# Optimization experiments

Measured on AMD Instinct MI355X. Metric: run time of the kernel, lower is better.

The kernel has to match this reference:

```python
import jax, jax.numpy as jnp
import numpy as np

BN_EPS = 1e-5


def setup_inputs() -> dict:
    key = jax.random.key(0)
    ks = jax.random.split(key, 5)
    b, c, h, w = 4, 128, 64, 64
    x = jax.random.normal(ks[0], (b, c, h, w), dtype=jnp.float32)
    # conv1x1 c -> 2c (fan-in scaled)
    w_inp = jax.random.normal(ks[1], (2 * c, c), dtype=jnp.float32) / np.sqrt(c)
    b_inp = jax.random.normal(ks[2], (2 * c,), dtype=jnp.float32) * 0.01
    bn_gamma = jnp.ones((2 * c,), dtype=jnp.float32)
    bn_beta = jnp.zeros((2 * c,), dtype=jnp.float32)
    bn_mean = jnp.zeros((2 * c,), dtype=jnp.float32)
    bn_var = jnp.ones((2 * c,), dtype=jnp.float32)
    w_out = jax.random.normal(ks[3], (c, c), dtype=jnp.float32) / np.sqrt(c)
    b_out = jax.random.normal(ks[4], (c,), dtype=jnp.float32) * 0.01
    return {
        "x": x, "w_inp": w_inp, "b_inp": b_inp,
        "bn_gamma": bn_gamma, "bn_beta": bn_beta,
        "bn_mean": bn_mean, "bn_var": bn_var,
        "w_out": w_out, "b_out": b_out,
    }


def reference(x, w_inp, b_inp, bn_gamma, bn_beta, bn_mean, bn_var, w_out, b_out):
    b, c, h, w = x.shape
    scale = c ** (-0.5)
    # project_inp: conv1x1 (c -> 2c) + BatchNorm2d (eval mode, running stats)
    t = jnp.einsum('bchw,oc->bohw', x, w_inp) + b_inp[None, :, None, None]
    bn_scale = bn_gamma * jax.lax.rsqrt(bn_var + BN_EPS)
    t = t * bn_scale[None, :, None, None] + (bn_beta - bn_mean * bn_scale)[None, :, None, None]
    # split qv along channels, flatten spatial to tokens: [b, N, c], N = h*w
    q = t[:, :c].reshape(b, c, h * w).transpose(0, 2, 1)
    v = t[:, c:].reshape(b, c, h * w).transpose(0, 2, 1)
    # self-similarity attention on q: [b, N, N]
    atn = jax.nn.softmax(jnp.einsum('bnc,bmc->bnm', q, q) * scale, axis=-1)
    y = jnp.einsum('bnm,bmc->bnc', atn, v)  # [b, N, c]
    y = y.transpose(0, 2, 1).reshape(b, c, h, w)
    # project_out: conv1x1 c -> c
    y = jnp.einsum('bchw,oc->bohw', y, w_out) + b_out[None, :, None, None]
    return (y, atn)
```

## Files before the change

kernel.cpp:

```cpp
#include <hip/hip_runtime.h>
#include <stdint.h>
#include <math.h>

#define C_DIM 128
#define N_TOK 4096
#define NB 4
#define LOG2E 1.4426950408889634f

typedef __attribute__((ext_vector_type(8))) short bf16x8;
typedef __attribute__((ext_vector_type(4))) short bf16x4;
typedef __attribute__((ext_vector_type(4))) float f32x4;

__device__ __forceinline__ unsigned short f2bf(float f) {
  unsigned u = __builtin_bit_cast(unsigned, f);
  unsigned r = (u + 0x7FFFu + ((u >> 16) & 1u)) >> 16;
  return (unsigned short)r;
}
__device__ __forceinline__ float bf2f(unsigned short h) {
  return __builtin_bit_cast(float, ((unsigned)h) << 16);
}
__device__ __forceinline__ void gload_lds16(const void* g, void* l) {
  __builtin_amdgcn_global_load_lds((const __attribute__((address_space(1))) void*)g,
                                   (__attribute__((address_space(3))) void*)l,
                                   16, 0, 0);
}

__global__ __launch_bounds__(256) void proj_in_kernel(
    const float* __restrict__ x, const float* __restrict__ w_inp,
    const float* __restrict__ b_inp, const float* __restrict__ gamma,
    const float* __restrict__ beta, const float* __restrict__ mean,
    const float* __restrict__ var,
    unsigned short* __restrict__ q, unsigned short* __restrict__ vT,
    int* __restrict__ m2bits) {
  __shared__ char smem[36096];
  unsigned short* xh = (unsigned short*)smem;
  unsigned short* xl = (unsigned short*)(smem + 17408);
  float* blkred = (float*)(smem + 35840);

  const int tid = threadIdx.x;
  const int b = blockIdx.x >> 6;
  const int n0 = (blockIdx.x & 63) << 6;
  const int lane = tid & 63;
  const int wave = tid >> 6;
  const int l15 = lane & 15, lg = lane >> 4;

  {
    const int c = tid >> 1;
    const int j0 = (tid & 1) * 32;
    const float* src = x + ((size_t)b * C_DIM + c) * N_TOK + n0 + j0;
#pragma unroll
    for (int j = 0; j < 32; j += 4) {
      float4 v4 = *(const float4*)(src + j);
#pragma unroll
      for (int e = 0; e < 4; e++) {
        float f = (&v4.x)[e];
        unsigned short hi = f2bf(f);
        unsigned short lo = f2bf(f - bf2f(hi));
        int n = j0 + j + e;
        xh[n * 136 + c] = hi;
        xl[n * 136 + c] = lo;
      }
    }
  }
  __syncthreads();

  f32x4 acc[4][4];
#pragma unroll
  for (int i = 0; i < 4; i++)
#pragma unroll
    for (int j = 0; j < 4; j++) acc[i][j] = {0.f, 0.f, 0.f, 0.f};

#pragma unroll
  for (int ks = 0; ks < 4; ks++) {
    bf16x8 ah[4], al[4];
#pragma unroll
    for (int ot = 0; ot < 4; ot++) {
      const int o = wave * 64 + ot * 16 + l15;
      const float* wp = w_inp + o * C_DIM + ks * 32 + lg * 8;
      float4 w0 = *(const float4*)wp;
      float4 w1 = *(const float4*)(wp + 4);
#pragma unroll
      for (int e = 0; e < 8; e++) {
        float f = (e < 4) ? (&w0.x)[e] : (&w1.x)[e - 4];
        unsigned short hi = f2bf(f);
        ah[ot][e] = (short)hi;
        al[ot][e] = (short)f2bf(f - bf2f(hi));
      }
    }
#pragma unroll
    for (int nt = 0; nt < 4; nt++) {
      const int off = (nt * 16 + l15) * 136 + ks * 32 + lg * 8;
      bf16x8 bh = *(const bf16x8*)(xh + off);
      bf16x8 bl = *(const bf16x8*)(xl + off);
#pragma unroll
      for (int ot = 0; ot < 4; ot++) {
        acc[ot][nt] = __builtin_amdgcn_mfma_f32_16x16x32_bf16(ah[ot], bh, acc[ot][nt], 0, 0, 0);
        acc[ot][nt] = __builtin_amdgcn_mfma_f32_16x16x32_bf16(ah[ot], bl, acc[ot][nt], 0, 0, 0);
        acc[ot][nt] = __builtin_amdgcn_mfma_f32_16x16x32_bf16(al[ot], bh, acc[ot][nt], 0, 0, 0);
      }
    }
  }
  __syncthreads();

  unsigned short* qT = (unsigned short*)smem;
  unsigned short* vTl = (unsigned short*)(smem + 17408);

#pragma unroll
  for (int ot = 0; ot < 4; ot++) {
#pragma unroll
    for (int r = 0; r < 4; r++) {
      const int o = wave * 64 + ot * 16 + lg * 4 + r;
      float A = gamma[o] * rsqrtf(var[o] + 1e-5f);
      float Bo = beta[o] + (b_inp[o] - mean[o]) * A;
#pragma unroll
      for (int nt = 0; nt < 4; nt++) {
        float val = acc[ot][nt][r] * A + Bo;
        unsigned short hv = f2bf(val);
        int n = nt * 16 + l15;
        if (wave < 2) {
          qT[n * 136 + o] = hv;
        } else {
          vTl[(o - 128) * 72 + n] = hv;
        }
      }
    }
  }
  __syncthreads();
  {
    int j = tid >> 2, c0 = (tid & 3) * 32;
    unsigned short* dst = q + ((size_t)b * N_TOK + n0 + j) * C_DIM + c0;
    const unsigned short* s = qT + j * 136 + c0;
#pragma unroll
    for (int i = 0; i < 32; i += 8) *(bf16x8*)(dst + i) = *(const bf16x8*)(s + i);
  }
  {
    int c = tid >> 1, h = (tid & 1) * 32;
    unsigned short* dst = vT + ((size_t)b * C_DIM + c) * N_TOK + n0 + h;
    const unsigned short* s = vTl + c * 72 + h;
#pragma unroll
    for (int i = 0; i < 32; i += 8) *(bf16x8*)(dst + i) = *(const bf16x8*)(s + i);
  }
  {
    int row = tid >> 2, qn = tid & 3;
    const unsigned short* qr = qT + row * 136 + qn * 32;
    float s = 0.f;
#pragma unroll
    for (int i = 0; i < 32; i++) {
      float f = bf2f(qr[i]);
      s = fmaf(f, f, s);
    }
    s += __shfl_xor(s, 1);
    s += __shfl_xor(s, 2);
    if ((tid & 3) == 0) blkred[row] = s;
    __syncthreads();
    if (tid < 64) {
      float v = blkred[tid];
      v = fmaxf(v, __shfl_xor(v, 1));
      v = fmaxf(v, __shfl_xor(v, 2));
      v = fmaxf(v, __shfl_xor(v, 4));
      v = fmaxf(v, __shfl_xor(v, 8));
      v = fmaxf(v, __shfl_xor(v, 16));
      v = fmaxf(v, __shfl_xor(v, 32));
      if (tid == 0) atomicMax(m2bits, __float_as_int(v));
    }
  }
}

__global__ __launch_bounds__(256) void attn_kernel(
    const unsigned short* __restrict__ q, const unsigned short* __restrict__ vT,
    const float* __restrict__ w_out, const float* __restrict__ b_out,
    float* __restrict__ yout, float* __restrict__ atn,
    const float* __restrict__ m2ptr) {
  __shared__ char smem[55552];

  const int tid = threadIdx.x;
  const int lane = tid & 63;
  const int wave = tid >> 6;
  const int rg = wave >> 1;
  const int kh = wave & 1;
  const int l15 = lane & 15, lg = lane >> 4, l7 = lane & 7;
  const int b = blockIdx.x >> 7;
  const int q0 = (blockIdx.x & 127) << 5;
  const int row0 = q0 + rg * 16;

  const unsigned short* qb = q + (size_t)b * N_TOK * C_DIM;
  const unsigned short* vb = vT + (size_t)b * C_DIM * N_TOK;

  const float scale = 0.08838834764831845f;
  const float ke = scale * LOG2E;
  const float nmk = -(m2ptr[0]) * ke;

  bf16x8 qf[4];
#pragma unroll
  for (int ks = 0; ks < 4; ks++)
    qf[ks] = *(const bf16x8*)(qb + (size_t)(row0 + l15) * C_DIM + ks * 32 + lg * 8);

  int koff[4];
#pragma unroll
  for (int ks = 0; ks < 4; ks++) koff[ks] = (ks * 64 + lg * 16) ^ (l7 * 16);
  const int krow = l15 * 256;

  auto stageK = [&](int kt, int buf) {
    char* base = smem + buf * 16384;
#pragma unroll
    for (int i = 0; i < 4; i++) {
      int lin = i * 256 + tid;
      int key = lin >> 4;
      int c = ((lin & 15) * 8) ^ ((key & 7) * 8);
      gload_lds16(qb + (size_t)(kt * 64 + key) * C_DIM + c, base + lin * 16);
    }
  };

  unsigned short* pbuf = (unsigned short*)(smem + 32768 + wave * 1280);
  float* statsL = (float*)(smem + 37888);
  float* ymergeF = (float*)(smem + 38144);

  const unsigned short* vlane = vb + (size_t)l15 * N_TOK + kh * 32 + lg * 8;

  float lpart = 0.f;
  f32x4 yacc[8];
#pragma unroll
  for (int ct = 0; ct < 8; ct++) yacc[ct] = {0.f, 0.f, 0.f, 0.f};

  bf16x8 vA[8], vB[8];
  stageK(0, 0);
#pragma unroll
  for (int ct = 0; ct < 8; ct++) vA[ct] = *(const bf16x8*)(vlane + (size_t)ct * 16 * N_TOK);
  __syncthreads();

  unsigned short* pbw0 = pbuf + l15 * 40 + lg * 4;
  unsigned short* pbw1 = pbuf + l15 * 40 + 16 + lg * 4;
  const unsigned short* par = pbuf + l15 * 40 + lg * 8;

  auto sweep1_iter = [&](int kt, bf16x8(&vc)[8], bf16x8(&vn)[8]) {
    if (kt + 1 < 64) {
      stageK(kt + 1, (kt + 1) & 1);
      const unsigned short* vp = vlane + (size_t)(kt + 1) * 64;
#pragma unroll
      for (int ct = 0; ct < 8; ct++) vn[ct] = *(const bf16x8*)(vp + (size_t)ct * 16 * N_TOK);
    }
    const char* kb = smem + (kt & 1) * 16384;
#pragma unroll
    for (int nt = 0; nt < 2; nt++) {
      f32x4 acc = {0.f, 0.f, 0.f, 0.f};
#pragma unroll
      for (int ks = 0; ks < 4; ks++) {
        bf16x8 ak = *(const bf16x8*)(kb + (kh * 2 + nt) * 4096 + krow + koff[ks]);
        acc = __builtin_amdgcn_mfma_f32_16x16x32_bf16(ak, qf[ks], acc, 0, 0, 0);
      }
      bf16x4 pk;
#pragma unroll
      for (int r = 0; r < 4; r++) {
        float p = __builtin_amdgcn_exp2f(fmaf(acc[r], ke, nmk));
        lpart += p;
        pk[r] = (short)f2bf(p);
      }
      *(bf16x4*)(nt ? pbw1 : pbw0) = pk;
    }
    bf16x8 ap = *(const bf16x8*)par;
#pragma unroll
    for (int ct = 0; ct < 8; ct++)
      yacc[ct] = __builtin_amdgcn_mfma_f32_16x16x32_bf16(ap, vc[ct], yacc[ct], 0, 0, 0);
    __syncthreads();
  };

  for (int kt = 0; kt < 64; kt += 2) {
    sweep1_iter(kt, vA, vB);
    sweep1_iter(kt + 1, vB, vA);
  }

  lpart += __shfl_xor(lpart, 16);
  lpart += __shfl_xor(lpart, 32);
  if (lg == 0) statsL[kh * 32 + rg * 16 + l15] = lpart;
  __syncthreads();

  float invl_r[4];
#pragma unroll
  for (int r = 0; r < 4; r++) {
    float ls = statsL[rg * 16 + lg * 4 + r] + statsL[32 + rg * 16 + lg * 4 + r];
    invl_r[r] = 1.0f / ls;
  }
  float invl2;
  {
    float ls = statsL[rg * 16 + l15] + statsL[32 + rg * 16 + l15];
    invl2 = 1.0f / ls;
  }

  if (kh) {
#pragma unroll
    for (int ct = 0; ct < 8; ct++)
#pragma unroll
      for (int r = 0; r < 4; r++)
        ymergeF[(rg * 16 + lg * 4 + r) * 136 + ct * 16 + l15] = yacc[ct][r];
  }
  __syncthreads();
  if (!kh) {
#pragma unroll
    for (int ct = 0; ct < 8; ct++)
#pragma unroll
      for (int r = 0; r < 4; r++)
        yacc[ct][r] = (yacc[ct][r] + ymergeF[(rg * 16 + lg * 4 + r) * 136 + ct * 16 + l15]) * invl_r[r];

    unsigned short* yl = (unsigned short*)(smem + rg * 16384);
    float* ol = (float*)(smem + rg * 16384 + 4608);
#pragma unroll
    for (int ct = 0; ct < 8; ct++)
#pragma unroll
      for (int r = 0; r < 4; r++)
        yl[(lg * 4 + r) * 136 + ct * 16 + l15] = f2bf(yacc[ct][r]);

    bf16x8 af[4];
#pragma unroll
    for (int ks = 0; ks < 4; ks++)
      af[ks] = *(const bf16x8*)(yl + l15 * 136 + ks * 32 + lg * 8);

#pragma unroll
    for (int cot = 0; cot < 8; cot++) {
      f32x4 oacc = {0.f, 0.f, 0.f, 0.f};
#pragma unroll
      for (int ks = 0; ks < 4; ks++) {
        const float* wp = w_out + (cot * 16 + l15) * C_DIM + ks * 32 + lg * 8;
        float4 w0 = *(const float4*)wp;
        float4 w1 = *(const float4*)(wp + 4);
        bf16x8 bw;
#pragma unroll
        for (int e = 0; e < 8; e++) bw[e] = (short)f2bf((e < 4) ? (&w0.x)[e] : (&w1.x)[e - 4]);
        oacc = __builtin_amdgcn_mfma_f32_16x16x32_bf16(af[ks], bw, oacc, 0, 0, 0);
      }
      float bo = b_out[cot * 16 + l15];
#pragma unroll
      for (int r = 0; r < 4; r++) ol[(cot * 16 + l15) * 20 + lg * 4 + r] = oacc[r] + bo;
    }
#pragma unroll
    for (int i = 0; i < 2; i++) {
      int co = i * 64 + lane;
      float* dst = yout + ((size_t)b * C_DIM + co) * N_TOK + row0;
      const float* s = ol + co * 20;
#pragma unroll
      for (int jj = 0; jj < 16; jj += 4) *(float4*)(dst + jj) = *(const float4*)(s + jj);
    }
  }
  __syncthreads();

  stageK(0, 0);
  __syncthreads();
  float* atnp = atn + ((size_t)b * N_TOK + row0 + l15) * N_TOK + kh * 32 + lg * 4;
  for (int kt = 0; kt < 64; kt++) {
    if (kt + 1 < 64) stageK(kt + 1, (kt + 1) & 1);
    const char* kb = smem + (kt & 1) * 16384;
#pragma unroll
    for (int nt = 0; nt < 2; nt++) {
      f32x4 acc = {0.f, 0.f, 0.f, 0.f};
#pragma unroll
      for (int ks = 0; ks < 4; ks++) {
        bf16x8 ak = *(const bf16x8*)(kb + (kh * 2 + nt) * 4096 + krow + koff[ks]);
        acc = __builtin_amdgcn_mfma_f32_16x16x32_bf16(ak, qf[ks], acc, 0, 0, 0);
      }
      float4 o;
#pragma unroll
      for (int r = 0; r < 4; r++)
        (&o.x)[r] = __builtin_amdgcn_exp2f(fmaf(acc[r], ke, nmk)) * invl2;
      *(float4*)(atnp + nt * 16) = o;
    }
    atnp += 64;
    __syncthreads();
  }
}

extern "C" void kernel_launch(void* const* d_in, const int* in_sizes, int n_in,
                              void* d_out, int out_size, void* d_ws, size_t ws_size,
                              hipStream_t stream) {
  const float* x = (const float*)d_in[0];
  const float* w_inp = (const float*)d_in[1];
  const float* b_inp = (const float*)d_in[2];
  const float* gamma = (const float*)d_in[3];
  const float* beta = (const float*)d_in[4];
  const float* mean = (const float*)d_in[5];
  const float* var = (const float*)d_in[6];
  const float* w_out = (const float*)d_in[7];
  const float* b_out = (const float*)d_in[8];

  float* out = (float*)d_out;
  float* yout = out;
  float* atn = out + (size_t)NB * C_DIM * N_TOK;

  unsigned short* q = (unsigned short*)d_ws;
  unsigned short* vT = q + (size_t)NB * N_TOK * C_DIM;
  int* m2bits = (int*)(vT + (size_t)NB * C_DIM * N_TOK);

  hipMemsetAsync(m2bits, 0, 4, stream);
  proj_in_kernel<<<256, 256, 0, stream>>>(x, w_inp, b_inp, gamma, beta, mean, var, q, vT, m2bits);
  attn_kernel<<<512, 256, 0, stream>>>(q, vT, w_out, b_out, yout, atn, (const float*)m2bits);
}
```

Baseline: 231.1 us.

## Load keys directly from global, stage attention output through LDS, remap block order

Removes the LDS double-buffered K staging (global_load_lds plus per-iteration barriers) and has each lane read its K fragments straight from global memory, relying on cache. The attention-matrix write pass now buffers four key tiles of probabilities in LDS and then writes full 1 KB row segments with coalesced float4 stores. Block indices are also swizzled so that blocks sharing a batch's K data are spread across the launch. This aims to cut barrier stalls and improve store coalescing for the large atn output, at the risk of more global/L2 traffic for K reads.

```diff
diff --git a/kernel.cpp b/kernel.cpp
--- a/kernel.cpp
+++ b/kernel.cpp
@@ -18,11 +18,6 @@
 }
 __device__ __forceinline__ float bf2f(unsigned short h) {
   return __builtin_bit_cast(float, ((unsigned)h) << 16);
-}
-__device__ __forceinline__ void gload_lds16(const void* g, void* l) {
-  __builtin_amdgcn_global_load_lds((const __attribute__((address_space(1))) void*)g,
-                                   (__attribute__((address_space(3))) void*)l,
-                                   16, 0, 0);
 }
 
 __global__ __launch_bounds__(256) void proj_in_kernel(
@@ -178,9 +173,10 @@
   const int wave = tid >> 6;
   const int rg = wave >> 1;
   const int kh = wave & 1;
-  const int l15 = lane & 15, lg = lane >> 4, l7 = lane & 7;
-  const int b = blockIdx.x >> 7;
-  const int q0 = (blockIdx.x & 127) << 5;
+  const int l15 = lane & 15, lg = lane >> 4;
+  const int bid = (int)((blockIdx.x & 7) * 64 + (blockIdx.x >> 3));
+  const int b = bid >> 7;
+  const int q0 = (bid & 127) << 5;
   const int row0 = q0 + rg * 16;
 
   const unsigned short* qb = q + (size_t)b * N_TOK * C_DIM;
@@ -195,25 +191,12 @@
   for (int ks = 0; ks < 4; ks++)
     qf[ks] = *(const bf16x8*)(qb + (size_t)(row0 + l15) * C_DIM + ks * 32 + lg * 8);
 
-  int koff[4];
-#pragma unroll
-  for (int ks = 0; ks < 4; ks++) koff[ks] = (ks * 64 + lg * 16) ^ (l7 * 16);
-  const int krow = l15 * 256;
-
-  auto stageK = [&](int kt, int buf) {
-    char* base = smem + buf * 16384;
-#pragma unroll
-    for (int i = 0; i < 4; i++) {
-      int lin = i * 256 + tid;
-      int key = lin >> 4;
-      int c = ((lin & 15) * 8) ^ ((key & 7) * 8);
-      gload_lds16(qb + (size_t)(kt * 64 + key) * C_DIM + c, base + lin * 16);
-    }
-  };
+  const unsigned short* kbase = qb + (size_t)(kh * 32 + l15) * C_DIM + lg * 8;
 
   unsigned short* pbuf = (unsigned short*)(smem + 32768 + wave * 1280);
   float* statsL = (float*)(smem + 37888);
   float* ymergeF = (float*)(smem + 38144);
+  float* sbuf = (float*)smem;
 
   const unsigned short* vlane = vb + (size_t)l15 * N_TOK + kh * 32 + lg * 8;
 
@@ -223,10 +206,8 @@
   for (int ct = 0; ct < 8; ct++) yacc[ct] = {0.f, 0.f, 0.f, 0.f};
 
   bf16x8 vA[8], vB[8];
-  stageK(0, 0);
 #pragma unroll
   for (int ct = 0; ct < 8; ct++) vA[ct] = *(const bf16x8*)(vlane + (size_t)ct * 16 * N_TOK);
-  __syncthreads();
 
   unsigned short* pbw0 = pbuf + l15 * 40 + lg * 4;
   unsigned short* pbw1 = pbuf + l15 * 40 + 16 + lg * 4;
@@ -234,18 +215,17 @@
 
   auto sweep1_iter = [&](int kt, bf16x8(&vc)[8], bf16x8(&vn)[8]) {
     if (kt + 1 < 64) {
-      stageK(kt + 1, (kt + 1) & 1);
       const unsigned short* vp = vlane + (size_t)(kt + 1) * 64;
 #pragma unroll
       for (int ct = 0; ct < 8; ct++) vn[ct] = *(const bf16x8*)(vp + (size_t)ct * 16 * N_TOK);
     }
-    const char* kb = smem + (kt & 1) * 16384;
+    const unsigned short* kp = kbase + (size_t)kt * 64 * C_DIM;
 #pragma unroll
     for (int nt = 0; nt < 2; nt++) {
       f32x4 acc = {0.f, 0.f, 0.f, 0.f};
 #pragma unroll
       for (int ks = 0; ks < 4; ks++) {
-        bf16x8 ak = *(const bf16x8*)(kb + (kh * 2 + nt) * 4096 + krow + koff[ks]);
+        bf16x8 ak = *(const bf16x8*)(kp + nt * 16 * C_DIM + ks * 32);
         acc = __builtin_amdgcn_mfma_f32_16x16x32_bf16(ak, qf[ks], acc, 0, 0, 0);
       }
       bf16x4 pk;
@@ -261,7 +241,6 @@
 #pragma unroll
     for (int ct = 0; ct < 8; ct++)
       yacc[ct] = __builtin_amdgcn_mfma_f32_16x16x32_bf16(ap, vc[ct], yacc[ct], 0, 0, 0);
-    __syncthreads();
   };
 
   for (int kt = 0; kt < 64; kt += 2) {
@@ -342,27 +321,38 @@
   }
   __syncthreads();
 
-  stageK(0, 0);
-  __syncthreads();
-  float* atnp = atn + ((size_t)b * N_TOK + row0 + l15) * N_TOK + kh * 32 + lg * 4;
-  for (int kt = 0; kt < 64; kt++) {
-    if (kt + 1 < 64) stageK(kt + 1, (kt + 1) & 1);
-    const char* kb = smem + (kt & 1) * 16384;
-#pragma unroll
-    for (int nt = 0; nt < 2; nt++) {
-      f32x4 acc = {0.f, 0.f, 0.f, 0.f};
-#pragma unroll
-      for (int ks = 0; ks < 4; ks++) {
-        bf16x8 ak = *(const bf16x8*)(kb + (kh * 2 + nt) * 4096 + krow + koff[ks]);
-        acc = __builtin_amdgcn_mfma_f32_16x16x32_bf16(ak, qf[ks], acc, 0, 0, 0);
-      }
-      float4 o;
-#pragma unroll
-      for (int r = 0; r < 4; r++)
-        (&o.x)[r] = __builtin_amdgcn_exp2f(fmaf(acc[r], ke, nmk)) * invl2;
-      *(float4*)(atnp + nt * 16) = o;
-    }
-    atnp += 64;
+  float* atnb2 = atn + ((size_t)b * N_TOK + q0) * N_TOK;
+  float* swr = sbuf + (size_t)(rg * 16 + l15) * 260 + kh * 32 + lg * 4;
+  for (int g = 0; g < 16; g++) {
+#pragma unroll
+    for (int j = 0; j < 4; j++) {
+      const int kt = g * 4 + j;
+      const unsigned short* kp = kbase + (size_t)kt * 64 * C_DIM;
+#pragma unroll
+      for (int nt = 0; nt < 2; nt++) {
+        f32x4 acc = {0.f, 0.f, 0.f, 0.f};
+#pragma unroll
+        for (int ks = 0; ks < 4; ks++) {
+          bf16x8 ak = *(const bf16x8*)(kp + nt * 16 * C_DIM + ks * 32);
+          acc = __builtin_amdgcn_mfma_f32_16x16x32_bf16(ak, qf[ks], acc, 0, 0, 0);
+        }
+        f32x4 o;
+#pragma unroll
+        for (int r = 0; r < 4; r++)
+          o[r] = __builtin_amdgcn_exp2f(fmaf(acc[r], ke, nmk)) * invl2;
+        *(f32x4*)(swr + j * 64 + nt * 16) = o;
+      }
+    }
+    __syncthreads();
+    {
+      const float* srcb = sbuf + (size_t)(wave * 8) * 260 + lane * 4;
+      float* dstb = atnb2 + (size_t)(wave * 8) * N_TOK + g * 256 + lane * 4;
+#pragma unroll
+      for (int rr = 0; rr < 8; rr++) {
+        f32x4 vv = *(const f32x4*)(srcb + (size_t)rr * 260);
+        *(f32x4*)(dstb + (size_t)rr * N_TOK) = vv;
+      }
+    }
     __syncthreads();
   }
 }
```

Result: slower. 390.8 us (+69.2%).

## Split attention work by key quarter per wave with 16-row blocks and smaller LDS

Applied to the files above, without the earlier changes.

Restructures the attention kernel so each block handles 16 query rows, with the four waves splitting the 64-key tile and the output channels (2 channel tiles each) instead of splitting rows and key halves. This cuts per-wave V registers and accumulators, shrinks LDS to allow 4 blocks per CU, doubles the grid to 1024 blocks, and swizzles block order. The P tile is now double-buffered in LDS and shared across waves, which costs an extra barrier dependency. The atn writes become nontemporal stores, and the output projection is split across waves.

```diff
diff --git a/kernel.cpp b/kernel.cpp
--- a/kernel.cpp
+++ b/kernel.cpp
@@ -166,22 +166,20 @@
   }
 }
 
-__global__ __launch_bounds__(256) void attn_kernel(
+__global__ __launch_bounds__(256, 4) void attn_kernel(
     const unsigned short* __restrict__ q, const unsigned short* __restrict__ vT,
     const float* __restrict__ w_out, const float* __restrict__ b_out,
     float* __restrict__ yout, float* __restrict__ atn,
     const float* __restrict__ m2ptr) {
-  __shared__ char smem[55552];
+  __shared__ char smem[37888];
 
   const int tid = threadIdx.x;
   const int lane = tid & 63;
-  const int wave = tid >> 6;
-  const int rg = wave >> 1;
-  const int kh = wave & 1;
+  const int kq = tid >> 6;
   const int l15 = lane & 15, lg = lane >> 4, l7 = lane & 7;
-  const int b = blockIdx.x >> 7;
-  const int q0 = (blockIdx.x & 127) << 5;
-  const int row0 = q0 + rg * 16;
+  const int bid = (int)((blockIdx.x & 7) * 128 + (blockIdx.x >> 3));
+  const int b = bid >> 8;
+  const int row0 = (bid & 255) << 4;
 
   const unsigned short* qb = q + (size_t)b * N_TOK * C_DIM;
   const unsigned short* vb = vT + (size_t)b * C_DIM * N_TOK;
@@ -198,7 +196,7 @@
   int koff[4];
 #pragma unroll
   for (int ks = 0; ks < 4; ks++) koff[ks] = (ks * 64 + lg * 16) ^ (l7 * 16);
-  const int krow = l15 * 256;
+  const int kqbase = kq * 4096 + l15 * 256;
 
   auto stageK = [&](int kt, int buf) {
     char* base = smem + buf * 16384;
@@ -211,57 +209,61 @@
     }
   };
 
-  unsigned short* pbuf = (unsigned short*)(smem + 32768 + wave * 1280);
-  float* statsL = (float*)(smem + 37888);
-  float* ymergeF = (float*)(smem + 38144);
-
-  const unsigned short* vlane = vb + (size_t)l15 * N_TOK + kh * 32 + lg * 8;
+  unsigned short* pbw = (unsigned short*)(smem + 32768) + l15 * 72 + kq * 16 + lg * 4;
+  const char* parb = smem + 32768 + l15 * 144;
+  float* statsL = (float*)(smem + 37376);
+
+  const unsigned short* vl0 = vb + (size_t)((kq * 2 + 0) * 16 + l15) * N_TOK + lg * 8;
+  const unsigned short* vl1 = vb + (size_t)((kq * 2 + 1) * 16 + l15) * N_TOK + lg * 8;
 
   float lpart = 0.f;
-  f32x4 yacc[8];
-#pragma unroll
-  for (int ct = 0; ct < 8; ct++) yacc[ct] = {0.f, 0.f, 0.f, 0.f};
-
-  bf16x8 vA[8], vB[8];
+  f32x4 yacc[2];
+  yacc[0] = {0.f, 0.f, 0.f, 0.f};
+  yacc[1] = {0.f, 0.f, 0.f, 0.f};
+
+  bf16x8 vA[2][2], vB[2][2];
   stageK(0, 0);
 #pragma unroll
-  for (int ct = 0; ct < 8; ct++) vA[ct] = *(const bf16x8*)(vlane + (size_t)ct * 16 * N_TOK);
-  __syncthreads();
-
-  unsigned short* pbw0 = pbuf + l15 * 40 + lg * 4;
-  unsigned short* pbw1 = pbuf + l15 * 40 + 16 + lg * 4;
-  const unsigned short* par = pbuf + l15 * 40 + lg * 8;
-
-  auto sweep1_iter = [&](int kt, bf16x8(&vc)[8], bf16x8(&vn)[8]) {
+  for (int ks2 = 0; ks2 < 2; ks2++) {
+    vA[0][ks2] = *(const bf16x8*)(vl0 + ks2 * 32);
+    vA[1][ks2] = *(const bf16x8*)(vl1 + ks2 * 32);
+  }
+  __syncthreads();
+
+  auto sweep1_iter = [&](int kt, bf16x8(&vc)[2][2], bf16x8(&vn)[2][2]) {
+    const char* kb = smem + (kt & 1) * 16384;
+    f32x4 acc = {0.f, 0.f, 0.f, 0.f};
+#pragma unroll
+    for (int ks = 0; ks < 4; ks++) {
+      bf16x8 ak = *(const bf16x8*)(kb + kqbase + koff[ks]);
+      acc = __builtin_amdgcn_mfma_f32_16x16x32_bf16(ak, qf[ks], acc, 0, 0, 0);
+    }
+    bf16x4 pk;
+#pragma unroll
+    for (int r = 0; r < 4; r++) {
+      float p = __builtin_amdgcn_exp2f(fmaf(acc[r], ke, nmk));
+      lpart += p;
+      pk[r] = (short)f2bf(p);
+    }
+    *(bf16x4*)(pbw + (kt & 1) * 1152) = pk;
+    if (kt + 1 < 64) stageK(kt + 1, (kt + 1) & 1);
+    __syncthreads();
+    const char* pbt = parb + (kt & 1) * 2304;
+#pragma unroll
+    for (int ks2 = 0; ks2 < 2; ks2++) {
+      bf16x8 ap = *(const bf16x8*)(pbt + ks2 * 64 + lg * 16);
+      yacc[0] = __builtin_amdgcn_mfma_f32_16x16x32_bf16(ap, vc[0][ks2], yacc[0], 0, 0, 0);
+      yacc[1] = __builtin_amdgcn_mfma_f32_16x16x32_bf16(ap, vc[1][ks2], yacc[1], 0, 0, 0);
+    }
     if (kt + 1 < 64) {
-      stageK(kt + 1, (kt + 1) & 1);
-      const unsigned short* vp = vlane + (size_t)(kt + 1) * 64;
-#pragma unroll
-      for (int ct = 0; ct < 8; ct++) vn[ct] = *(const bf16x8*)(vp + (size_t)ct * 16 * N_TOK);
-    }
-    const char* kb = smem + (kt & 1) * 16384;
-#pragma unroll
-    for (int nt = 0; nt < 2; nt++) {
-      f32x4 acc = {0.f, 0.f, 0.f, 0.f};
-#pragma unroll
-      for (int ks = 0; ks < 4; ks++) {
-        bf16x8 ak = *(const bf16x8*)(kb + (kh * 2 + nt) * 4096 + krow + koff[ks]);
-        acc = __builtin_amdgcn_mfma_f32_16x16x32_bf16(ak, qf[ks], acc, 0, 0, 0);
-      }
-      bf16x4 pk;
-#pragma unroll
-      for (int r = 0; r < 4; r++) {
-        float p = __builtin_amdgcn_exp2f(fmaf(acc[r], ke, nmk));
-        lpart += p;
-        pk[r] = (short)f2bf(p);
-      }
-      *(bf16x4*)(nt ? pbw1 : pbw0) = pk;
-    }
-    bf16x8 ap = *(const bf16x8*)par;
-#pragma unroll
-    for (int ct = 0; ct < 8; ct++)
-      yacc[ct] = __builtin_amdgcn_mfma_f32_16x16x32_bf16(ap, vc[ct], yacc[ct], 0, 0, 0);
-    __syncthreads();
+      const unsigned short* v0 = vl0 + (size_t)(kt + 1) * 64;
+      const unsigned short* v1 = vl1 + (size_t)(kt + 1) * 64;
+#pragma unroll
+      for (int ks2 = 0; ks2 < 2; ks2++) {
+        vn[0][ks2] = *(const bf16x8*)(v0 + ks2 * 32);
+        vn[1][ks2] = *(const bf16x8*)(v1 + ks2 * 32);
+      }
+    }
   };
 
   for (int kt = 0; kt < 64; kt += 2) {
@@ -271,43 +273,28 @@
 
   lpart += __shfl_xor(lpart, 16);
   lpart += __shfl_xor(lpart, 32);
-  if (lg == 0) statsL[kh * 32 + rg * 16 + l15] = lpart;
+  if (lg == 0) statsL[kq * 16 + l15] = lpart;
   __syncthreads();
 
   float invl_r[4];
 #pragma unroll
   for (int r = 0; r < 4; r++) {
-    float ls = statsL[rg * 16 + lg * 4 + r] + statsL[32 + rg * 16 + lg * 4 + r];
-    invl_r[r] = 1.0f / ls;
-  }
-  float invl2;
-  {
-    float ls = statsL[rg * 16 + l15] + statsL[32 + rg * 16 + l15];
-    invl2 = 1.0f / ls;
-  }
-
-  if (kh) {
-#pragma unroll
-    for (int ct = 0; ct < 8; ct++)
+    const int row = lg * 4 + r;
+    invl_r[r] = 1.0f / (statsL[row] + statsL[16 + row] + statsL[32 + row] + statsL[48 + row]);
+  }
+  const float invl2 =
+      1.0f / (statsL[l15] + statsL[16 + l15] + statsL[32 + l15] + statsL[48 + l15]);
+
+  __syncthreads();
+  {
+    unsigned short* yl = (unsigned short*)smem;
+    float* ol = (float*)(smem + 8192);
+#pragma unroll
+    for (int ctl = 0; ctl < 2; ctl++)
 #pragma unroll
       for (int r = 0; r < 4; r++)
-        ymergeF[(rg * 16 + lg * 4 + r) * 136 + ct * 16 + l15] = yacc[ct][r];
-  }
-  __syncthreads();
-  if (!kh) {
-#pragma unroll
-    for (int ct = 0; ct < 8; ct++)
-#pragma unroll
-      for (int r = 0; r < 4; r++)
-        yacc[ct][r] = (yacc[ct][r] + ymergeF[(rg * 16 + lg * 4 + r) * 136 + ct * 16 + l15]) * invl_r[r];
-
-    unsigned short* yl = (unsigned short*)(smem + rg * 16384);
-    float* ol = (float*)(smem + rg * 16384 + 4608);
-#pragma unroll
-    for (int ct = 0; ct < 8; ct++)
-#pragma unroll
-      for (int r = 0; r < 4; r++)
-        yl[(lg * 4 + r) * 136 + ct * 16 + l15] = f2bf(yacc[ct][r]);
+        yl[(lg * 4 + r) * 136 + (kq * 2 + ctl) * 16 + l15] = f2bf(yacc[ctl][r] * invl_r[r]);
+    __syncthreads();
 
     bf16x8 af[4];
 #pragma unroll
@@ -315,7 +302,8 @@
       af[ks] = *(const bf16x8*)(yl + l15 * 136 + ks * 32 + lg * 8);
 
 #pragma unroll
-    for (int cot = 0; cot < 8; cot++) {
+    for (int cotl = 0; cotl < 2; cotl++) {
+      const int cot = kq * 2 + cotl;
       f32x4 oacc = {0.f, 0.f, 0.f, 0.f};
 #pragma unroll
       for (int ks = 0; ks < 4; ks++) {
@@ -331,38 +319,35 @@
 #pragma unroll
       for (int r = 0; r < 4; r++) ol[(cot * 16 + l15) * 20 + lg * 4 + r] = oacc[r] + bo;
     }
-#pragma unroll
-    for (int i = 0; i < 2; i++) {
-      int co = i * 64 + lane;
-      float* dst = yout + ((size_t)b * C_DIM + co) * N_TOK + row0;
-      const float* s = ol + co * 20;
-#pragma unroll
-      for (int jj = 0; jj < 16; jj += 4) *(float4*)(dst + jj) = *(const float4*)(s + jj);
+    __syncthreads();
+    {
+      const int co = tid >> 1;
+      const int r0 = (tid & 1) * 8;
+      float* dst = yout + ((size_t)b * C_DIM + co) * N_TOK + row0 + r0;
+      const float* s = ol + co * 20 + r0;
+      *(float4*)dst = *(const float4*)s;
+      *(float4*)(dst + 4) = *(const float4*)(s + 4);
     }
   }
   __syncthreads();
 
   stageK(0, 0);
   __syncthreads();
-  float* atnp = atn + ((size_t)b * N_TOK + row0 + l15) * N_TOK + kh * 32 + lg * 4;
+  float* atnp = atn + ((size_t)b * N_TOK + row0 + l15) * N_TOK + kq * 16 + lg * 4;
   for (int kt = 0; kt < 64; kt++) {
+    const char* kb = smem + (kt & 1) * 16384;
+    f32x4 acc = {0.f, 0.f, 0.f, 0.f};
+#pragma unroll
+    for (int ks = 0; ks < 4; ks++) {
+      bf16x8 ak = *(const bf16x8*)(kb + kqbase + koff[ks]);
+      acc = __builtin_amdgcn_mfma_f32_16x16x32_bf16(ak, qf[ks], acc, 0, 0, 0);
+    }
+    f32x4 o;
+#pragma unroll
+    for (int r = 0; r < 4; r++)
+      o[r] = __builtin_amdgcn_exp2f(fmaf(acc[r], ke, nmk)) * invl2;
+    __builtin_nontemporal_store(o, (f32x4*)(atnp + (size_t)kt * 64));
     if (kt + 1 < 64) stageK(kt + 1, (kt + 1) & 1);
-    const char* kb = smem + (kt & 1) * 16384;
-#pragma unroll
-    for (int nt = 0; nt < 2; nt++) {
-      f32x4 acc = {0.f, 0.f, 0.f, 0.f};
-#pragma unroll
-      for (int ks = 0; ks < 4; ks++) {
-        bf16x8 ak = *(const bf16x8*)(kb + (kh * 2 + nt) * 4096 + krow + koff[ks]);
-        acc = __builtin_amdgcn_mfma_f32_16x16x32_bf16(ak, qf[ks], acc, 0, 0, 0);
-      }
-      float4 o;
-#pragma unroll
-      for (int r = 0; r < 4; r++)
-        (&o.x)[r] = __builtin_amdgcn_exp2f(fmaf(acc[r], ke, nmk)) * invl2;
-      *(float4*)(atnp + nt * 16) = o;
-    }
-    atnp += 64;
     __syncthreads();
   }
 }
@@ -390,5 +375,5 @@
 
   hipMemsetAsync(m2bits, 0, 4, stream);
   proj_in_kernel<<<256, 256, 0, stream>>>(x, w_inp, b_inp, gamma, beta, mean, var, q, vT, m2bits);
-  attn_kernel<<<512, 256, 0, stream>>>(q, vT, w_out, b_out, yout, atn, (const float*)m2bits);
-}
+  attn_kernel<<<1024, 256, 0, stream>>>(q, vT, w_out, b_out, yout, atn, (const float*)m2bits);
+}
```

After: 250.6 us. +8.5%, slower.

## Split attention-matrix write into separate tiled kernel and relax PV loop syncs

Applied to the files above, without the earlier changes.

Moves the second sweep that recomputes and writes the full normalized attention matrix out of the PV kernel into a new kernel that tiles 128x128 blocks across 4096 workgroups. Row inverse sums are passed through workspace. The PV loop replaces __syncthreads with a manual vmcnt wait plus barrier, and both kernels use an XCD-aware block remap and a 2-blocks-per-CU occupancy hint. The goal is more parallelism and better store throughput for the dominant 256 MB atn write, at the cost of one extra launch and recomputing QK^T in the new kernel.

```diff
diff --git a/kernel.cpp b/kernel.cpp
--- a/kernel.cpp
+++ b/kernel.cpp
@@ -10,6 +10,10 @@
 typedef __attribute__((ext_vector_type(8))) short bf16x8;
 typedef __attribute__((ext_vector_type(4))) short bf16x4;
 typedef __attribute__((ext_vector_type(4))) float f32x4;
+
+#define WAIT_VM(N) asm volatile("s_waitcnt vmcnt(" #N ")" ::: "memory")
+#define SBAR() __builtin_amdgcn_s_barrier()
+#define SCHED_FENCE() __builtin_amdgcn_sched_barrier(0)
 
 __device__ __forceinline__ unsigned short f2bf(float f) {
   unsigned u = __builtin_bit_cast(unsigned, f);
@@ -166,10 +170,10 @@
   }
 }
 
-__global__ __launch_bounds__(256) void attn_kernel(
+__global__ __launch_bounds__(256, 2) void attn_pv_kernel(
     const unsigned short* __restrict__ q, const unsigned short* __restrict__ vT,
     const float* __restrict__ w_out, const float* __restrict__ b_out,
-    float* __restrict__ yout, float* __restrict__ atn,
+    float* __restrict__ yout, float* __restrict__ invlw,
     const float* __restrict__ m2ptr) {
   __shared__ char smem[55552];
 
@@ -179,8 +183,9 @@
   const int rg = wave >> 1;
   const int kh = wave & 1;
   const int l15 = lane & 15, lg = lane >> 4, l7 = lane & 7;
-  const int b = blockIdx.x >> 7;
-  const int q0 = (blockIdx.x & 127) << 5;
+  const int bid = (int)((blockIdx.x & 7) * 64 + (blockIdx.x >> 3));
+  const int b = bid >> 7;
+  const int q0 = (bid & 127) << 5;
   const int row0 = q0 + rg * 16;
 
   const unsigned short* qb = q + (size_t)b * N_TOK * C_DIM;
@@ -226,19 +231,22 @@
   stageK(0, 0);
 #pragma unroll
   for (int ct = 0; ct < 8; ct++) vA[ct] = *(const bf16x8*)(vlane + (size_t)ct * 16 * N_TOK);
-  __syncthreads();
 
   unsigned short* pbw0 = pbuf + l15 * 40 + lg * 4;
   unsigned short* pbw1 = pbuf + l15 * 40 + 16 + lg * 4;
   const unsigned short* par = pbuf + l15 * 40 + lg * 8;
 
   auto sweep1_iter = [&](int kt, bf16x8(&vc)[8], bf16x8(&vn)[8]) {
+    WAIT_VM(8);
+    SBAR();
+    SCHED_FENCE();
     if (kt + 1 < 64) {
       stageK(kt + 1, (kt + 1) & 1);
       const unsigned short* vp = vlane + (size_t)(kt + 1) * 64;
 #pragma unroll
       for (int ct = 0; ct < 8; ct++) vn[ct] = *(const bf16x8*)(vp + (size_t)ct * 16 * N_TOK);
     }
+    SCHED_FENCE();
     const char* kb = smem + (kt & 1) * 16384;
 #pragma unroll
     for (int nt = 0; nt < 2; nt++) {
@@ -261,29 +269,26 @@
 #pragma unroll
     for (int ct = 0; ct < 8; ct++)
       yacc[ct] = __builtin_amdgcn_mfma_f32_16x16x32_bf16(ap, vc[ct], yacc[ct], 0, 0, 0);
-    __syncthreads();
   };
 
   for (int kt = 0; kt < 64; kt += 2) {
     sweep1_iter(kt, vA, vB);
     sweep1_iter(kt + 1, vB, vA);
   }
+  WAIT_VM(0);
 
   lpart += __shfl_xor(lpart, 16);
   lpart += __shfl_xor(lpart, 32);
   if (lg == 0) statsL[kh * 32 + rg * 16 + l15] = lpart;
   __syncthreads();
 
+  if (tid < 32) invlw[(size_t)b * N_TOK + q0 + tid] = 1.0f / (statsL[tid] + statsL[32 + tid]);
+
   float invl_r[4];
 #pragma unroll
   for (int r = 0; r < 4; r++) {
-    float ls = statsL[rg * 16 + lg * 4 + r] + statsL[32 + rg * 16 + lg * 4 + r];
-    invl_r[r] = 1.0f / ls;
-  }
-  float invl2;
-  {
-    float ls = statsL[rg * 16 + l15] + statsL[32 + rg * 16 + l15];
-    invl2 = 1.0f / ls;
+    const int row = lg * 4 + r;
+    invl_r[r] = 1.0f / (statsL[rg * 16 + row] + statsL[32 + rg * 16 + row]);
   }
 
   if (kh) {
@@ -340,30 +345,87 @@
       for (int jj = 0; jj < 16; jj += 4) *(float4*)(dst + jj) = *(const float4*)(s + jj);
     }
   }
-  __syncthreads();
-
-  stageK(0, 0);
-  __syncthreads();
-  float* atnp = atn + ((size_t)b * N_TOK + row0 + l15) * N_TOK + kh * 32 + lg * 4;
-  for (int kt = 0; kt < 64; kt++) {
-    if (kt + 1 < 64) stageK(kt + 1, (kt + 1) & 1);
-    const char* kb = smem + (kt & 1) * 16384;
-#pragma unroll
-    for (int nt = 0; nt < 2; nt++) {
-      f32x4 acc = {0.f, 0.f, 0.f, 0.f};
-#pragma unroll
-      for (int ks = 0; ks < 4; ks++) {
-        bf16x8 ak = *(const bf16x8*)(kb + (kh * 2 + nt) * 4096 + krow + koff[ks]);
-        acc = __builtin_amdgcn_mfma_f32_16x16x32_bf16(ak, qf[ks], acc, 0, 0, 0);
-      }
-      float4 o;
-#pragma unroll
-      for (int r = 0; r < 4; r++)
-        (&o.x)[r] = __builtin_amdgcn_exp2f(fmaf(acc[r], ke, nmk)) * invl2;
-      *(float4*)(atnp + nt * 16) = o;
-    }
-    atnp += 64;
-    __syncthreads();
+}
+
+__global__ __launch_bounds__(256, 2) void atn_write_kernel(
+    const unsigned short* __restrict__ q, const float* __restrict__ invl,
+    float* __restrict__ atn, const float* __restrict__ m2ptr) {
+  __shared__ char smem[65536];
+
+  const int tid = threadIdx.x;
+  const int lane = tid & 63;
+  const int wv = tid >> 6;
+  const int l15 = lane & 15, lg = lane >> 4, l7 = lane & 7;
+  const int bid = (int)((blockIdx.x & 7) * 512 + (blockIdx.x >> 3));
+  const int b = bid >> 10;
+  const int rem = bid & 1023;
+  const int n0 = ((rem >> 5) & 31) << 7;
+  const int m0 = (rem & 31) << 7;
+
+  const unsigned short* qb = q + (size_t)b * N_TOK * C_DIM;
+  const float ke = 0.08838834764831845f * LOG2E;
+  const float nmk = -(m2ptr[0]) * ke;
+
+#pragma unroll
+  for (int i = 0; i < 8; i++) {
+    int lin = i * 256 + tid;
+    int row = lin >> 4;
+    int c = ((lin & 15) * 8) ^ ((row & 7) * 8);
+    gload_lds16(qb + (size_t)(n0 + row) * C_DIM + c, smem + lin * 16);
+  }
+#pragma unroll
+  for (int i = 0; i < 8; i++) {
+    int lin = i * 256 + tid;
+    int row = lin >> 4;
+    int c = ((lin & 15) * 8) ^ ((row & 7) * 8);
+    gload_lds16(qb + (size_t)(m0 + row) * C_DIM + c, smem + 32768 + lin * 16);
+  }
+
+  float iv[8];
+#pragma unroll
+  for (int nt = 0; nt < 8; nt++) iv[nt] = invl[(size_t)b * N_TOK + n0 + nt * 16 + l15];
+
+  WAIT_VM(0);
+  SBAR();
+
+  int koff[4];
+#pragma unroll
+  for (int ks = 0; ks < 4; ks++) koff[ks] = (ks * 64 + lg * 16) ^ (l7 * 16);
+  const char* qt = smem;
+  const char* ktl = smem + 32768;
+  const int wm = wv * 32;
+
+  bf16x8 am[2][4];
+#pragma unroll
+  for (int mt = 0; mt < 2; mt++)
+#pragma unroll
+    for (int ks = 0; ks < 4; ks++)
+      am[mt][ks] = *(const bf16x8*)(ktl + (wm + mt * 16 + l15) * 256 + koff[ks]);
+
+  float* atnb = atn + ((size_t)b * N_TOK + n0) * N_TOK + m0 + wm;
+
+#pragma unroll
+  for (int nt = 0; nt < 8; nt++) {
+    bf16x8 bq[4];
+#pragma unroll
+    for (int ks = 0; ks < 4; ks++)
+      bq[ks] = *(const bf16x8*)(qt + (nt * 16 + l15) * 256 + koff[ks]);
+    f32x4 acc0 = {0.f, 0.f, 0.f, 0.f};
+    f32x4 acc1 = {0.f, 0.f, 0.f, 0.f};
+#pragma unroll
+    for (int ks = 0; ks < 4; ks++) {
+      acc0 = __builtin_amdgcn_mfma_f32_16x16x32_bf16(am[0][ks], bq[ks], acc0, 0, 0, 0);
+      acc1 = __builtin_amdgcn_mfma_f32_16x16x32_bf16(am[1][ks], bq[ks], acc1, 0, 0, 0);
+    }
+    float* rowp = atnb + (size_t)(nt * 16 + l15) * N_TOK + lg * 4;
+    f32x4 o0, o1;
+#pragma unroll
+    for (int r = 0; r < 4; r++) {
+      o0[r] = __builtin_amdgcn_exp2f(fmaf(acc0[r], ke, nmk)) * iv[nt];
+      o1[r] = __builtin_amdgcn_exp2f(fmaf(acc1[r], ke, nmk)) * iv[nt];
+    }
+    *(f32x4*)rowp = o0;
+    *(f32x4*)(rowp + 16) = o1;
   }
 }
 
@@ -386,9 +448,12 @@
 
   unsigned short* q = (unsigned short*)d_ws;
   unsigned short* vT = q + (size_t)NB * N_TOK * C_DIM;
-  int* m2bits = (int*)(vT + (size_t)NB * C_DIM * N_TOK);
+  char* after = (char*)(vT + (size_t)NB * C_DIM * N_TOK);
+  int* m2bits = (int*)after;
+  float* invlw = (float*)(after + 256);
 
   hipMemsetAsync(m2bits, 0, 4, stream);
   proj_in_kernel<<<256, 256, 0, stream>>>(x, w_inp, b_inp, gamma, beta, mean, var, q, vT, m2bits);
-  attn_kernel<<<512, 256, 0, stream>>>(q, vT, w_out, b_out, yout, atn, (const float*)m2bits);
-}
+  attn_pv_kernel<<<512, 256, 0, stream>>>(q, vT, w_out, b_out, yout, invlw, (const float*)m2bits);
+  atn_write_kernel<<<4096, 256, 0, stream>>>(q, invlw, atn, (const float*)m2bits);
+}
```

After: 225.5 us. 2.4% less time.
